# Kernel tuning notes

Hardware: AMD Instinct MI355X
Metric: run time of the kernel (lower is better)

## Reference

```python
import jax, jax.numpy as jnp
import numpy as np

TOP_K = 4  # num_experts_per_tok


def setup_inputs() -> dict:
    key = jax.random.key(0)
    ks = jax.random.split(key, 7)
    B, S, H, E, I = 1, 1024, 1024, 16, 2880
    scale_h = 1.0 / np.sqrt(H)
    scale_i = 1.0 / np.sqrt(I)
    return {
        "hidden_states": jax.random.normal(ks[0], (B, S, H), jnp.float32),
        "gate_w": jax.random.normal(ks[1], (E, H), jnp.float32) * scale_h,
        "gate_b": jax.random.normal(ks[2], (E,), jnp.float32) * 0.01,
        "gate_up_proj": jax.random.normal(ks[3], (E, H, 2 * I), jnp.float32) * scale_h,
        "gate_up_proj_bias": jax.random.normal(ks[4], (E, 2 * I), jnp.float32) * 0.01,
        "down_proj": jax.random.normal(ks[5], (E, I, H), jnp.float32) * scale_i,
        "down_proj_bias": jax.random.normal(ks[6], (E, H), jnp.float32) * 0.01,
    }


def reference(hidden_states, gate_w, gate_b, gate_up_proj, gate_up_proj_bias,
              down_proj, down_proj_bias):
    B, S, H = hidden_states.shape
    E = gate_w.shape[0]
    I = down_proj.shape[1]
    x = hidden_states.reshape(-1, H)  # [T, H]
    T = x.shape[0]

    # Router: top-k logits, softmax over selected logits only
    router_logits = x @ gate_w.T + gate_b          # [T, E]
    top_vals, top_idx = jax.lax.top_k(router_logits, TOP_K)
    routing_weights = jax.nn.softmax(top_vals, axis=-1)  # [T, K]

    # Combine matrix: C[t, e] = routing weight of expert e for token t (0 if unselected)
    C = jnp.zeros((T, E), x.dtype).at[jnp.arange(T)[:, None], top_idx].add(routing_weights)

    # Dense per-expert MLP (reference computes all experts, combine masks unselected)
    gu = jnp.einsum('th,ehf->tef', x, gate_up_proj) + gate_up_proj_bias[None]  # [T, E, 2I]
    gate, up = gu[..., :I], gu[..., I:]
    inter = jax.nn.silu(gate) * up                                            # [T, E, I]
    expert_out = jnp.einsum('tei,eih->teh', inter, down_proj) + down_proj_bias[None]  # [T, E, H]
    out = jnp.einsum('teh,te->th', expert_out, C)                             # [T, H]

    return out.reshape(B, S, H), router_logits
```

## Files before the change

### kernel.cpp

```cpp
#include <hip/hip_runtime.h>
#include <hip/hip_bf16.h>
#include <stdint.h>

#define T_TOK 1024
#define HDIM  1024
#define NEXP  16
#define IDIM  2880
#define GU_COLS (2*IDIM)
#define TOPK  4

using short4v  = __attribute__((ext_vector_type(4))) short;
using short8   = __attribute__((ext_vector_type(8))) short;
using ushort4v = __attribute__((ext_vector_type(4))) unsigned short;
using f32x4    = __attribute__((ext_vector_type(4))) float;

__device__ __forceinline__ unsigned short f2b(float f) {
    union { float f; unsigned u; } x; x.f = f;
    unsigned r = x.u + 0x7FFFu + ((x.u >> 16) & 1u);
    return (unsigned short)(r >> 16);
}

typedef const __attribute__((address_space(1))) unsigned int* gas1_t;
typedef __attribute__((address_space(3))) unsigned int* las3_t;
__device__ __forceinline__ void gload16(const void* g, void* l) {
    __builtin_amdgcn_global_load_lds((gas1_t)g, (las3_t)l, 16, 0, 0);
}

__global__ __launch_bounds__(256) void router_kernel(
    const float* __restrict__ x, const float* __restrict__ gw,
    const float* __restrict__ gb, float* __restrict__ logits_out,
    int* __restrict__ counts, int* __restrict__ lists, float* __restrict__ wts,
    unsigned short* __restrict__ xb, float* __restrict__ out)
{
    int t = blockIdx.x;
    int tid = threadIdx.x;
    const float* xr = x + (size_t)t * HDIM;
    {
        float4 v = *(const float4*)(xr + tid * 4);
        ushort4v b; b.x = f2b(v.x); b.y = f2b(v.y); b.z = f2b(v.z); b.w = f2b(v.w);
        *(ushort4v*)(xb + (size_t)t * HDIM + tid * 4) = b;
        float4 z = make_float4(0.f, 0.f, 0.f, 0.f);
        *(float4*)(out + (size_t)t * HDIM + tid * 4) = z;
    }
    int e = tid >> 4;
    int l16 = tid & 15;
    const float* wr = gw + (size_t)e * HDIM;
    float p = 0.f;
    for (int h = l16; h < HDIM; h += 16) p += xr[h] * wr[h];
    p += __shfl_xor(p, 8);
    p += __shfl_xor(p, 4);
    p += __shfl_xor(p, 2);
    p += __shfl_xor(p, 1);
    __shared__ float sl[NEXP];
    if (l16 == 0) {
        float v = p + gb[e];
        sl[e] = v;
        logits_out[t * NEXP + e] = v;
    }
    __syncthreads();
    if (tid == 0) {
        float v[NEXP];
#pragma unroll
        for (int i = 0; i < NEXP; ++i) v[i] = sl[i];
        int idx[TOPK]; float tv[TOPK];
        unsigned used = 0;
#pragma unroll
        for (int k = 0; k < TOPK; ++k) {
            float best = -__builtin_inff(); int bi = 0;
#pragma unroll
            for (int i = 0; i < NEXP; ++i)
                if (!((used >> i) & 1u) && v[i] > best) { best = v[i]; bi = i; }
            used |= 1u << bi; idx[k] = bi; tv[k] = best;
        }
        float m = tv[0];
        float ex[TOPK], s = 0.f;
#pragma unroll
        for (int k = 0; k < TOPK; ++k) { ex[k] = expf(tv[k] - m); s += ex[k]; }
#pragma unroll
        for (int k = 0; k < TOPK; ++k) {
            float w = ex[k] / s;
            int slot = atomicAdd(&counts[idx[k]], 1);
            lists[idx[k] * T_TOK + slot] = t;
            wts[idx[k] * T_TOK + slot] = w;
        }
    }
}

__global__ void offsets_kernel(const int* __restrict__ counts, int* __restrict__ offsets)
{
    if (threadIdx.x == 0) {
        int o = 0;
        for (int e = 0; e < NEXP; ++e) { offsets[e] = o; o += counts[e]; }
        offsets[NEXP] = o;
    }
}

__global__ __launch_bounds__(512) void gu_kernel(
    const unsigned short* __restrict__ xb, const float* __restrict__ gup,
    const float* __restrict__ gub, const int* __restrict__ counts,
    const int* __restrict__ offsets, const int* __restrict__ lists,
    unsigned short* __restrict__ inter)
{
    int bid = blockIdx.x;
    int nt = bid % 90;
    int t2 = bid / 90;
    int e  = t2 & 15;
    int mt = t2 >> 4;
    int ne = counts[e];
    if (mt * 256 >= ne) return;

    int tid = threadIdx.x;
    int wave = tid >> 6, lane = tid & 63;
    int l16 = lane & 15, lq = lane >> 4;

    __shared__ int tokid[256];
    __shared__ unsigned short As[256 * 64];
    __shared__ unsigned short Bs[64 * 64];

    if (tid < 256) {
        int slot = mt * 256 + tid;
        tokid[tid] = (slot < ne) ? lists[e * T_TOK + slot] : lists[e * T_TOK];
    }
    __syncthreads();

    const float* gup_e = gup + (size_t)e * HDIM * GU_COLS;

    int at = tid - 256;
    const unsigned short* asrc[8];
    if (tid >= 256) {
#pragma unroll
        for (int i = 0; i < 8; ++i) {
            int s = at + i * 256;
            int row = s >> 3, c = s & 7;
            asrc[i] = xb + (size_t)tokid[row] * HDIM + ((c ^ (row & 7)) * 8);
        }
    }
    int nb = tid & 15, kb = tid >> 4;
    const float* bsrc = nullptr;
    if (tid < 256) {
        int n0 = nb * 4;
        size_t col = (n0 < 32) ? (size_t)(nt * 32 + n0) : (size_t)(IDIM + nt * 32 + (n0 - 32));
        bsrc = gup_e + (size_t)(kb * 4) * GU_COLS + col;
    }

    f32x4 acc[2][4];
#pragma unroll
    for (int i = 0; i < 2; ++i)
#pragma unroll
        for (int f = 0; f < 4; ++f) acc[i][f] = (f32x4){0.f, 0.f, 0.f, 0.f};

    float4 br0, br1, br2, br3;
    if (tid < 256) {
        br0 = *(const float4*)(bsrc);
        br1 = *(const float4*)(bsrc + GU_COLS);
        br2 = *(const float4*)(bsrc + 2 * GU_COLS);
        br3 = *(const float4*)(bsrc + 3 * GU_COLS);
    }

    for (int kk = 0; kk < HDIM; kk += 64) {
        __syncthreads();
        if (tid >= 256) {
#pragma unroll
            for (int i = 0; i < 8; ++i)
                gload16(asrc[i] + kk, As + ((size_t)(at + i * 256)) * 8);
        } else {
#pragma unroll
            for (int j = 0; j < 4; ++j) {
                int n = nb * 4 + j;
                int slot = kb ^ (n & 15);
                ushort4v b;
                b.x = f2b((&br0.x)[j]); b.y = f2b((&br1.x)[j]);
                b.z = f2b((&br2.x)[j]); b.w = f2b((&br3.x)[j]);
                *(ushort4v*)&Bs[n * 64 + slot * 4] = b;
            }
        }
        __syncthreads();
        if (tid < 256 && kk + 64 < HDIM) {
            const float* sp = bsrc + (size_t)(kk + 64) * GU_COLS;
            br0 = *(const float4*)(sp);
            br1 = *(const float4*)(sp + GU_COLS);
            br2 = *(const float4*)(sp + 2 * GU_COLS);
            br3 = *(const float4*)(sp + 3 * GU_COLS);
        }
#pragma unroll
        for (int ks = 0; ks < 2; ++ks) {
            short8 a[2], b[4];
#pragma unroll
            for (int i = 0; i < 2; ++i) {
                int row = wave * 32 + i * 16 + l16;
                int q = ks * 4 + lq;
                a[i] = *(const short8*)&As[row * 64 + ((q ^ (row & 7)) * 8)];
            }
#pragma unroll
            for (int f = 0; f < 4; ++f) {
                int n = f * 16 + l16;
                int u0 = (ks * 8 + lq * 2) ^ (n & 15);
                int u1 = (ks * 8 + lq * 2 + 1) ^ (n & 15);
                short4v h0 = *(const short4v*)&Bs[n * 64 + u0 * 4];
                short4v h1 = *(const short4v*)&Bs[n * 64 + u1 * 4];
                b[f] = __builtin_shufflevector(h0, h1, 0, 1, 2, 3, 4, 5, 6, 7);
            }
#pragma unroll
            for (int i = 0; i < 2; ++i)
#pragma unroll
                for (int f = 0; f < 4; ++f)
                    acc[i][f] = __builtin_amdgcn_mfma_f32_16x16x32_bf16(a[i], b[f], acc[i][f], 0, 0, 0);
        }
    }

    int off = offsets[e];
    const float* gbe = gub + (size_t)e * GU_COLS;
#pragma unroll
    for (int j = 0; j < 2; ++j) {
        int col = j * 16 + l16;
        float bg = gbe[nt * 32 + col];
        float bu = gbe[IDIM + nt * 32 + col];
#pragma unroll
        for (int i = 0; i < 2; ++i)
#pragma unroll
            for (int r = 0; r < 4; ++r) {
                int row = wave * 32 + i * 16 + lq * 4 + r;
                int slot = mt * 256 + row;
                if (slot < ne) {
                    float g = acc[i][j][r] + bg;
                    float u = acc[i][j + 2][r] + bu;
                    float sg = g / (1.f + expf(-g));
                    inter[(size_t)(off + slot) * IDIM + nt * 32 + col] = f2b(sg * u);
                }
            }
    }
}

__global__ __launch_bounds__(512) void down_kernel(
    const unsigned short* __restrict__ inter, const float* __restrict__ dw,
    const float* __restrict__ db, const int* __restrict__ counts,
    const int* __restrict__ offsets, const int* __restrict__ lists,
    const float* __restrict__ wts, float* __restrict__ out)
{
    int bid = blockIdx.x;
    int ht = bid & 15;
    int t2 = bid >> 4;
    int e  = t2 & 15;
    int mt = t2 >> 4;
    int ne = counts[e];
    if (mt * 256 >= ne) return;

    int tid = threadIdx.x;
    int wave = tid >> 6, lane = tid & 63;
    int l16 = lane & 15, lq = lane >> 4;

    __shared__ int tokid[256];
    __shared__ float twt[256];
    __shared__ unsigned short As[256 * 64];
    __shared__ unsigned short Bs[64 * 64];

    int off = offsets[e];
    if (tid < 256) {
        int slot = mt * 256 + tid;
        tokid[tid] = (slot < ne) ? lists[e * T_TOK + slot] : -1;
        twt[tid]   = (slot < ne) ? wts[e * T_TOK + slot] : 0.f;
    }
    __syncthreads();

    const float* dw_e = dw + (size_t)e * IDIM * HDIM;

    int at = tid - 256;
    const unsigned short* asrc[8];
    if (tid >= 256) {
#pragma unroll
        for (int i = 0; i < 8; ++i) {
            int s = at + i * 256;
            int row = s >> 3, c = s & 7;
            int slotr = mt * 256 + row; if (slotr >= ne) slotr = ne - 1;
            asrc[i] = inter + (size_t)(off + slotr) * IDIM + ((c ^ (row & 7)) * 8);
        }
    }
    int nb = tid & 15, kb = tid >> 4;
    const float* bsrc = nullptr;
    if (tid < 256)
        bsrc = dw_e + (size_t)(kb * 4) * HDIM + ht * 64 + nb * 4;

    f32x4 acc[2][4];
#pragma unroll
    for (int i = 0; i < 2; ++i)
#pragma unroll
        for (int f = 0; f < 4; ++f) acc[i][f] = (f32x4){0.f, 0.f, 0.f, 0.f};

    float4 br0, br1, br2, br3;
    if (tid < 256) {
        br0 = *(const float4*)(bsrc);
        br1 = *(const float4*)(bsrc + HDIM);
        br2 = *(const float4*)(bsrc + 2 * HDIM);
        br3 = *(const float4*)(bsrc + 3 * HDIM);
    }

    for (int kk = 0; kk < IDIM; kk += 64) {
        __syncthreads();
        if (tid >= 256) {
#pragma unroll
            for (int i = 0; i < 8; ++i)
                gload16(asrc[i] + kk, As + ((size_t)(at + i * 256)) * 8);
        } else {
#pragma unroll
            for (int j = 0; j < 4; ++j) {
                int n = nb * 4 + j;
                int slot = kb ^ (n & 15);
                ushort4v b;
                b.x = f2b((&br0.x)[j]); b.y = f2b((&br1.x)[j]);
                b.z = f2b((&br2.x)[j]); b.w = f2b((&br3.x)[j]);
                *(ushort4v*)&Bs[n * 64 + slot * 4] = b;
            }
        }
        __syncthreads();
        if (tid < 256 && kk + 64 < IDIM) {
            const float* sp = bsrc + (size_t)(kk + 64) * HDIM;
            br0 = *(const float4*)(sp);
            br1 = *(const float4*)(sp + HDIM);
            br2 = *(const float4*)(sp + 2 * HDIM);
            br3 = *(const float4*)(sp + 3 * HDIM);
        }
#pragma unroll
        for (int ks = 0; ks < 2; ++ks) {
            short8 a[2], b[4];
#pragma unroll
            for (int i = 0; i < 2; ++i) {
                int row = wave * 32 + i * 16 + l16;
                int q = ks * 4 + lq;
                a[i] = *(const short8*)&As[row * 64 + ((q ^ (row & 7)) * 8)];
            }
#pragma unroll
            for (int f = 0; f < 4; ++f) {
                int n = f * 16 + l16;
                int u0 = (ks * 8 + lq * 2) ^ (n & 15);
                int u1 = (ks * 8 + lq * 2 + 1) ^ (n & 15);
                short4v h0 = *(const short4v*)&Bs[n * 64 + u0 * 4];
                short4v h1 = *(const short4v*)&Bs[n * 64 + u1 * 4];
                b[f] = __builtin_shufflevector(h0, h1, 0, 1, 2, 3, 4, 5, 6, 7);
            }
#pragma unroll
            for (int i = 0; i < 2; ++i)
#pragma unroll
                for (int f = 0; f < 4; ++f)
                    acc[i][f] = __builtin_amdgcn_mfma_f32_16x16x32_bf16(a[i], b[f], acc[i][f], 0, 0, 0);
        }
    }

    const float* db_e = db + (size_t)e * HDIM;
#pragma unroll
    for (int f = 0; f < 4; ++f) {
        int h = ht * 64 + f * 16 + l16;
        float bias = db_e[h];
#pragma unroll
        for (int i = 0; i < 2; ++i)
#pragma unroll
            for (int r = 0; r < 4; ++r) {
                int row = wave * 32 + i * 16 + lq * 4 + r;
                int tk = tokid[row];
                if (tk >= 0)
                    atomicAdd(out + (size_t)tk * HDIM + h, twt[row] * (acc[i][f][r] + bias));
            }
    }
}

extern "C" void kernel_launch(void* const* d_in, const int* in_sizes, int n_in,
                              void* d_out, int out_size, void* d_ws, size_t ws_size,
                              hipStream_t stream)
{
    const float* x   = (const float*)d_in[0];
    const float* gw  = (const float*)d_in[1];
    const float* gb  = (const float*)d_in[2];
    const float* gup = (const float*)d_in[3];
    const float* gub = (const float*)d_in[4];
    const float* dw  = (const float*)d_in[5];
    const float* db  = (const float*)d_in[6];

    float* out        = (float*)d_out;
    float* logits_out = out + (size_t)T_TOK * HDIM;

    char* ws = (char*)d_ws;
    int*   counts  = (int*)(ws + 0);
    int*   offsets = (int*)(ws + 256);
    int*   lists   = (int*)(ws + 512);
    float* wts     = (float*)(ws + 512 + 65536);
    unsigned short* xb    = (unsigned short*)(ws + 131584);
    unsigned short* inter = (unsigned short*)(ws + 2228736);

    hipMemsetAsync(counts, 0, 64, stream);

    router_kernel<<<T_TOK, 256, 0, stream>>>(x, gw, gb, logits_out, counts, lists, wts, xb, out);
    offsets_kernel<<<1, 64, 0, stream>>>(counts, offsets);
    gu_kernel<<<4 * NEXP * 90, 512, 0, stream>>>(xb, gup, gub, counts, offsets, lists, inter);
    down_kernel<<<4 * NEXP * 16, 512, 0, stream>>>(inter, dw, db, counts, offsets, lists, wts, out);
}
```

Before: 307.5 us.

## Double N-tile width in MoE GEMMs to 128 with 4x2 wave layout

Widens the per-block N tile from 64 to 128 columns in both the gate/up and down expert GEMMs. Waves are rearranged into a 4x2 grid so each computes a 64x64 sub-tile, which halves the grid size and the number of times the gathered activation tile is reloaded. Raises MFMA priority around the compute loop with s_setprio. In exchange it uses more accumulator registers and LDS per block and launches fewer blocks, which can lower occupancy and leave some CUs idle.

```diff
diff --git a/kernel.cpp b/kernel.cpp
--- a/kernel.cpp
+++ b/kernel.cpp
@@ -102,8 +102,8 @@
     unsigned short* __restrict__ inter)
 {
     int bid = blockIdx.x;
-    int nt = bid % 90;
-    int t2 = bid / 90;
+    int nt = bid % 45;
+    int t2 = bid / 45;
     int e  = t2 & 15;
     int mt = t2 >> 4;
     int ne = counts[e];
@@ -112,10 +112,11 @@
     int tid = threadIdx.x;
     int wave = tid >> 6, lane = tid & 63;
     int l16 = lane & 15, lq = lane >> 4;
+    int wm = wave >> 1, wn = wave & 1;
 
     __shared__ int tokid[256];
     __shared__ unsigned short As[256 * 64];
-    __shared__ unsigned short Bs[64 * 64];
+    __shared__ unsigned short Bs[128 * 64];
 
     if (tid < 256) {
         int slot = mt * 256 + tid;
@@ -136,25 +137,31 @@
         }
     }
     int nb = tid & 15, kb = tid >> 4;
-    const float* bsrc = nullptr;
-    if (tid < 256) {
-        int n0 = nb * 4;
-        size_t col = (n0 < 32) ? (size_t)(nt * 32 + n0) : (size_t)(IDIM + nt * 32 + (n0 - 32));
-        bsrc = gup_e + (size_t)(kb * 4) * GU_COLS + col;
-    }
-
-    f32x4 acc[2][4];
-#pragma unroll
-    for (int i = 0; i < 2; ++i)
+    const float* bsrcg[2];
+    if (tid < 256) {
+#pragma unroll
+        for (int t = 0; t < 2; ++t) {
+            int n0 = (nb + t * 16) * 4;
+            int is_up = (n0 >> 5) & 1;
+            int cw = (n0 & 31) + ((n0 >> 6) << 5);
+            size_t gcol = (is_up ? (size_t)IDIM : 0) + (size_t)nt * 64 + cw;
+            bsrcg[t] = gup_e + (size_t)(kb * 4) * GU_COLS + gcol;
+        }
+    }
+
+    f32x4 acc[4][4];
+#pragma unroll
+    for (int i = 0; i < 4; ++i)
 #pragma unroll
         for (int f = 0; f < 4; ++f) acc[i][f] = (f32x4){0.f, 0.f, 0.f, 0.f};
 
-    float4 br0, br1, br2, br3;
-    if (tid < 256) {
-        br0 = *(const float4*)(bsrc);
-        br1 = *(const float4*)(bsrc + GU_COLS);
-        br2 = *(const float4*)(bsrc + 2 * GU_COLS);
-        br3 = *(const float4*)(bsrc + 3 * GU_COLS);
+    float4 br[2][4];
+    if (tid < 256) {
+#pragma unroll
+        for (int t = 0; t < 2; ++t)
+#pragma unroll
+            for (int k = 0; k < 4; ++k)
+                br[t][k] = *(const float4*)(bsrcg[t] + (size_t)k * GU_COLS);
     }
 
     for (int kk = 0; kk < HDIM; kk += 64) {
@@ -165,67 +172,71 @@
                 gload16(asrc[i] + kk, As + ((size_t)(at + i * 256)) * 8);
         } else {
 #pragma unroll
-            for (int j = 0; j < 4; ++j) {
-                int n = nb * 4 + j;
-                int slot = kb ^ (n & 15);
-                ushort4v b;
-                b.x = f2b((&br0.x)[j]); b.y = f2b((&br1.x)[j]);
-                b.z = f2b((&br2.x)[j]); b.w = f2b((&br3.x)[j]);
-                *(ushort4v*)&Bs[n * 64 + slot * 4] = b;
-            }
+            for (int t = 0; t < 2; ++t)
+#pragma unroll
+                for (int j = 0; j < 4; ++j) {
+                    int n = (nb + t * 16) * 4 + j;
+                    int slot = kb ^ (n & 15);
+                    ushort4v b;
+                    b.x = f2b((&br[t][0].x)[j]); b.y = f2b((&br[t][1].x)[j]);
+                    b.z = f2b((&br[t][2].x)[j]); b.w = f2b((&br[t][3].x)[j]);
+                    *(ushort4v*)&Bs[n * 64 + slot * 4] = b;
+                }
         }
         __syncthreads();
         if (tid < 256 && kk + 64 < HDIM) {
-            const float* sp = bsrc + (size_t)(kk + 64) * GU_COLS;
-            br0 = *(const float4*)(sp);
-            br1 = *(const float4*)(sp + GU_COLS);
-            br2 = *(const float4*)(sp + 2 * GU_COLS);
-            br3 = *(const float4*)(sp + 3 * GU_COLS);
-        }
+#pragma unroll
+            for (int t = 0; t < 2; ++t)
+#pragma unroll
+                for (int k = 0; k < 4; ++k)
+                    br[t][k] = *(const float4*)(bsrcg[t] + (size_t)(kk + 64 + k) * GU_COLS);
+        }
+        __builtin_amdgcn_s_setprio(1);
 #pragma unroll
         for (int ks = 0; ks < 2; ++ks) {
-            short8 a[2], b[4];
-#pragma unroll
-            for (int i = 0; i < 2; ++i) {
-                int row = wave * 32 + i * 16 + l16;
+            short8 a[4], b[4];
+#pragma unroll
+            for (int i = 0; i < 4; ++i) {
+                int row = wm * 64 + i * 16 + l16;
                 int q = ks * 4 + lq;
                 a[i] = *(const short8*)&As[row * 64 + ((q ^ (row & 7)) * 8)];
             }
 #pragma unroll
             for (int f = 0; f < 4; ++f) {
-                int n = f * 16 + l16;
-                int u0 = (ks * 8 + lq * 2) ^ (n & 15);
-                int u1 = (ks * 8 + lq * 2 + 1) ^ (n & 15);
+                int n = wn * 64 + f * 16 + l16;
+                int u0 = (ks * 8 + lq * 2) ^ l16;
+                int u1 = (ks * 8 + lq * 2 + 1) ^ l16;
                 short4v h0 = *(const short4v*)&Bs[n * 64 + u0 * 4];
                 short4v h1 = *(const short4v*)&Bs[n * 64 + u1 * 4];
                 b[f] = __builtin_shufflevector(h0, h1, 0, 1, 2, 3, 4, 5, 6, 7);
             }
 #pragma unroll
-            for (int i = 0; i < 2; ++i)
+            for (int i = 0; i < 4; ++i)
 #pragma unroll
                 for (int f = 0; f < 4; ++f)
                     acc[i][f] = __builtin_amdgcn_mfma_f32_16x16x32_bf16(a[i], b[f], acc[i][f], 0, 0, 0);
         }
+        __builtin_amdgcn_s_setprio(0);
     }
 
     int off = offsets[e];
     const float* gbe = gub + (size_t)e * GU_COLS;
 #pragma unroll
     for (int j = 0; j < 2; ++j) {
-        int col = j * 16 + l16;
-        float bg = gbe[nt * 32 + col];
-        float bu = gbe[IDIM + nt * 32 + col];
-#pragma unroll
-        for (int i = 0; i < 2; ++i)
+        int cw = wn * 32 + j * 16 + l16;
+        float bg = gbe[nt * 64 + cw];
+        float bu = gbe[IDIM + nt * 64 + cw];
+#pragma unroll
+        for (int i = 0; i < 4; ++i)
 #pragma unroll
             for (int r = 0; r < 4; ++r) {
-                int row = wave * 32 + i * 16 + lq * 4 + r;
+                int row = wm * 64 + i * 16 + lq * 4 + r;
                 int slot = mt * 256 + row;
                 if (slot < ne) {
                     float g = acc[i][j][r] + bg;
                     float u = acc[i][j + 2][r] + bu;
                     float sg = g / (1.f + expf(-g));
-                    inter[(size_t)(off + slot) * IDIM + nt * 32 + col] = f2b(sg * u);
+                    inter[(size_t)(off + slot) * IDIM + nt * 64 + cw] = f2b(sg * u);
                 }
             }
     }
@@ -238,8 +249,8 @@
     const float* __restrict__ wts, float* __restrict__ out)
 {
     int bid = blockIdx.x;
-    int ht = bid & 15;
-    int t2 = bid >> 4;
+    int ht = bid & 7;
+    int t2 = bid >> 3;
     int e  = t2 & 15;
     int mt = t2 >> 4;
     int ne = counts[e];
@@ -248,11 +259,12 @@
     int tid = threadIdx.x;
     int wave = tid >> 6, lane = tid & 63;
     int l16 = lane & 15, lq = lane >> 4;
+    int wm = wave >> 1, wn = wave & 1;
 
     __shared__ int tokid[256];
     __shared__ float twt[256];
     __shared__ unsigned short As[256 * 64];
-    __shared__ unsigned short Bs[64 * 64];
+    __shared__ unsigned short Bs[128 * 64];
 
     int off = offsets[e];
     if (tid < 256) {
@@ -276,22 +288,26 @@
         }
     }
     int nb = tid & 15, kb = tid >> 4;
-    const float* bsrc = nullptr;
-    if (tid < 256)
-        bsrc = dw_e + (size_t)(kb * 4) * HDIM + ht * 64 + nb * 4;
-
-    f32x4 acc[2][4];
-#pragma unroll
-    for (int i = 0; i < 2; ++i)
+    const float* bsrcg[2];
+    if (tid < 256) {
+#pragma unroll
+        for (int t = 0; t < 2; ++t)
+            bsrcg[t] = dw_e + (size_t)(kb * 4) * HDIM + ht * 128 + (nb + t * 16) * 4;
+    }
+
+    f32x4 acc[4][4];
+#pragma unroll
+    for (int i = 0; i < 4; ++i)
 #pragma unroll
         for (int f = 0; f < 4; ++f) acc[i][f] = (f32x4){0.f, 0.f, 0.f, 0.f};
 
-    float4 br0, br1, br2, br3;
-    if (tid < 256) {
-        br0 = *(const float4*)(bsrc);
-        br1 = *(const float4*)(bsrc + HDIM);
-        br2 = *(const float4*)(bsrc + 2 * HDIM);
-        br3 = *(const float4*)(bsrc + 3 * HDIM);
+    float4 br[2][4];
+    if (tid < 256) {
+#pragma unroll
+        for (int t = 0; t < 2; ++t)
+#pragma unroll
+            for (int k = 0; k < 4; ++k)
+                br[t][k] = *(const float4*)(bsrcg[t] + (size_t)k * HDIM);
     }
 
     for (int kk = 0; kk < IDIM; kk += 64) {
@@ -302,59 +318,63 @@
                 gload16(asrc[i] + kk, As + ((size_t)(at + i * 256)) * 8);
         } else {
 #pragma unroll
-            for (int j = 0; j < 4; ++j) {
-                int n = nb * 4 + j;
-                int slot = kb ^ (n & 15);
-                ushort4v b;
-                b.x = f2b((&br0.x)[j]); b.y = f2b((&br1.x)[j]);
-                b.z = f2b((&br2.x)[j]); b.w = f2b((&br3.x)[j]);
-                *(ushort4v*)&Bs[n * 64 + slot * 4] = b;
-            }
+            for (int t = 0; t < 2; ++t)
+#pragma unroll
+                for (int j = 0; j < 4; ++j) {
+                    int n = (nb + t * 16) * 4 + j;
+                    int slot = kb ^ (n & 15);
+                    ushort4v b;
+                    b.x = f2b((&br[t][0].x)[j]); b.y = f2b((&br[t][1].x)[j]);
+                    b.z = f2b((&br[t][2].x)[j]); b.w = f2b((&br[t][3].x)[j]);
+                    *(ushort4v*)&Bs[n * 64 + slot * 4] = b;
+                }
         }
         __syncthreads();
         if (tid < 256 && kk + 64 < IDIM) {
-            const float* sp = bsrc + (size_t)(kk + 64) * HDIM;
-            br0 = *(const float4*)(sp);
-            br1 = *(const float4*)(sp + HDIM);
-            br2 = *(const float4*)(sp + 2 * HDIM);
-            br3 = *(const float4*)(sp + 3 * HDIM);
-        }
+#pragma unroll
+            for (int t = 0; t < 2; ++t)
+#pragma unroll
+                for (int k = 0; k < 4; ++k)
+                    br[t][k] = *(const float4*)(bsrcg[t] + (size_t)(kk + 64 + k) * HDIM);
+        }
+        __builtin_amdgcn_s_setprio(1);
 #pragma unroll
         for (int ks = 0; ks < 2; ++ks) {
-            short8 a[2], b[4];
-#pragma unroll
-            for (int i = 0; i < 2; ++i) {
-                int row = wave * 32 + i * 16 + l16;
+            short8 a[4], b[4];
+#pragma unroll
+            for (int i = 0; i < 4; ++i) {
+                int row = wm * 64 + i * 16 + l16;
                 int q = ks * 4 + lq;
                 a[i] = *(const short8*)&As[row * 64 + ((q ^ (row & 7)) * 8)];
             }
 #pragma unroll
             for (int f = 0; f < 4; ++f) {
-                int n = f * 16 + l16;
-                int u0 = (ks * 8 + lq * 2) ^ (n & 15);
-                int u1 = (ks * 8 + lq * 2 + 1) ^ (n & 15);
+                int n = wn * 64 + f * 16 + l16;
+                int u0 = (ks * 8 + lq * 2) ^ l16;
+                int u1 = (ks * 8 + lq * 2 + 1) ^ l16;
                 short4v h0 = *(const short4v*)&Bs[n * 64 + u0 * 4];
                 short4v h1 = *(const short4v*)&Bs[n * 64 + u1 * 4];
                 b[f] = __builtin_shufflevector(h0, h1, 0, 1, 2, 3, 4, 5, 6, 7);
             }
 #pragma unroll
-            for (int i = 0; i < 2; ++i)
+            for (int i = 0; i < 4; ++i)
 #pragma unroll
                 for (int f = 0; f < 4; ++f)
                     acc[i][f] = __builtin_amdgcn_mfma_f32_16x16x32_bf16(a[i], b[f], acc[i][f], 0, 0, 0);
         }
+        __builtin_amdgcn_s_setprio(0);
     }
 
     const float* db_e = db + (size_t)e * HDIM;
 #pragma unroll
     for (int f = 0; f < 4; ++f) {
-        int h = ht * 64 + f * 16 + l16;
+        int h = ht * 128 + wn * 64 + f * 16 + l16;
         float bias = db_e[h];
 #pragma unroll
-        for (int i = 0; i < 2; ++i)
+        for (int i = 0; i < 4; ++i)
 #pragma unroll
             for (int r = 0; r < 4; ++r) {
-                int row = wave * 32 + i * 16 + lq * 4 + r;
+                int row = wm * 64 + i * 16 + lq * 4 + r;
                 int tk = tokid[row];
                 if (tk >= 0)
                     atomicAdd(out + (size_t)tk * HDIM + h, twt[row] * (acc[i][f][r] + bias));
@@ -389,6 +409,6 @@
 
     router_kernel<<<T_TOK, 256, 0, stream>>>(x, gw, gb, logits_out, counts, lists, wts, xb, out);
     offsets_kernel<<<1, 64, 0, stream>>>(counts, offsets);
-    gu_kernel<<<4 * NEXP * 90, 512, 0, stream>>>(xb, gup, gub, counts, offsets, lists, inter);
-    down_kernel<<<4 * NEXP * 16, 512, 0, stream>>>(inter, dw, db, counts, offsets, lists, wts, out);
-}
+    gu_kernel<<<4 * NEXP * 45, 512, 0, stream>>>(xb, gup, gub, counts, offsets, lists, inter);
+    down_kernel<<<4 * NEXP * 8, 512, 0, stream>>>(inter, dw, db, counts, offsets, lists, wts, out);
+}
```

New measurement: 346.9 us. 12.8% more time.

## Split down-proj K dimension across two blocks, widen LDS B reads, raise MFMA priority

Applied to the files above, without the earlier changes.

The down-projection kernel now splits the 2880-long reduction into two halves handled by separate blocks, doubling the grid. Both halves accumulate into the output with atomics, and only the first half adds the bias. The aim is more parallelism for the down GEMM, at the cost of twice as many output atomics and duplicate A-tile loads per block. The B-tile swizzle is changed to XOR with (n&14) so each lane can fetch its B fragment with one 16-byte LDS read instead of two 8-byte reads. s_setprio is raised around the MFMA section in both GEMM kernels.

```diff
diff --git a/kernel.cpp b/kernel.cpp
--- a/kernel.cpp
+++ b/kernel.cpp
@@ -9,7 +9,6 @@
 #define GU_COLS (2*IDIM)
 #define TOPK  4
 
-using short4v  = __attribute__((ext_vector_type(4))) short;
 using short8   = __attribute__((ext_vector_type(8))) short;
 using ushort4v = __attribute__((ext_vector_type(4))) unsigned short;
 using f32x4    = __attribute__((ext_vector_type(4))) float;
@@ -167,7 +166,7 @@
 #pragma unroll
             for (int j = 0; j < 4; ++j) {
                 int n = nb * 4 + j;
-                int slot = kb ^ (n & 15);
+                int slot = kb ^ (n & 14);
                 ushort4v b;
                 b.x = f2b((&br0.x)[j]); b.y = f2b((&br1.x)[j]);
                 b.z = f2b((&br2.x)[j]); b.w = f2b((&br3.x)[j]);
@@ -182,6 +181,7 @@
             br2 = *(const float4*)(sp + 2 * GU_COLS);
             br3 = *(const float4*)(sp + 3 * GU_COLS);
         }
+        __builtin_amdgcn_s_setprio(1);
 #pragma unroll
         for (int ks = 0; ks < 2; ++ks) {
             short8 a[2], b[4];
@@ -194,11 +194,8 @@
 #pragma unroll
             for (int f = 0; f < 4; ++f) {
                 int n = f * 16 + l16;
-                int u0 = (ks * 8 + lq * 2) ^ (n & 15);
-                int u1 = (ks * 8 + lq * 2 + 1) ^ (n & 15);
-                short4v h0 = *(const short4v*)&Bs[n * 64 + u0 * 4];
-                short4v h1 = *(const short4v*)&Bs[n * 64 + u1 * 4];
-                b[f] = __builtin_shufflevector(h0, h1, 0, 1, 2, 3, 4, 5, 6, 7);
+                int u = (ks * 8 + lq * 2) ^ (n & 14);
+                b[f] = *(const short8*)&Bs[n * 64 + u * 4];
             }
 #pragma unroll
             for (int i = 0; i < 2; ++i)
@@ -206,6 +203,7 @@
                 for (int f = 0; f < 4; ++f)
                     acc[i][f] = __builtin_amdgcn_mfma_f32_16x16x32_bf16(a[i], b[f], acc[i][f], 0, 0, 0);
         }
+        __builtin_amdgcn_s_setprio(0);
     }
 
     int off = offsets[e];
@@ -238,12 +236,15 @@
     const float* __restrict__ wts, float* __restrict__ out)
 {
     int bid = blockIdx.x;
-    int ht = bid & 15;
-    int t2 = bid >> 4;
-    int e  = t2 & 15;
-    int mt = t2 >> 4;
+    int ht  = bid & 15;
+    int e   = (bid >> 4) & 15;
+    int ksp = (bid >> 8) & 1;
+    int mt  = bid >> 9;
     int ne = counts[e];
     if (mt * 256 >= ne) return;
+
+    int k0   = ksp * 1472;
+    int kend = ksp ? IDIM : 1472;
 
     int tid = threadIdx.x;
     int wave = tid >> 6, lane = tid & 63;
@@ -288,13 +289,14 @@
 
     float4 br0, br1, br2, br3;
     if (tid < 256) {
-        br0 = *(const float4*)(bsrc);
-        br1 = *(const float4*)(bsrc + HDIM);
-        br2 = *(const float4*)(bsrc + 2 * HDIM);
-        br3 = *(const float4*)(bsrc + 3 * HDIM);
-    }
-
-    for (int kk = 0; kk < IDIM; kk += 64) {
+        const float* sp = bsrc + (size_t)k0 * HDIM;
+        br0 = *(const float4*)(sp);
+        br1 = *(const float4*)(sp + HDIM);
+        br2 = *(const float4*)(sp + 2 * HDIM);
+        br3 = *(const float4*)(sp + 3 * HDIM);
+    }
+
+    for (int kk = k0; kk < kend; kk += 64) {
         __syncthreads();
         if (tid >= 256) {
 #pragma unroll
@@ -304,7 +306,7 @@
 #pragma unroll
             for (int j = 0; j < 4; ++j) {
                 int n = nb * 4 + j;
-                int slot = kb ^ (n & 15);
+                int slot = kb ^ (n & 14);
                 ushort4v b;
                 b.x = f2b((&br0.x)[j]); b.y = f2b((&br1.x)[j]);
                 b.z = f2b((&br2.x)[j]); b.w = f2b((&br3.x)[j]);
@@ -312,13 +314,14 @@
             }
         }
         __syncthreads();
-        if (tid < 256 && kk + 64 < IDIM) {
+        if (tid < 256 && kk + 64 < kend) {
             const float* sp = bsrc + (size_t)(kk + 64) * HDIM;
             br0 = *(const float4*)(sp);
             br1 = *(const float4*)(sp + HDIM);
             br2 = *(const float4*)(sp + 2 * HDIM);
             br3 = *(const float4*)(sp + 3 * HDIM);
         }
+        __builtin_amdgcn_s_setprio(1);
 #pragma unroll
         for (int ks = 0; ks < 2; ++ks) {
             short8 a[2], b[4];
@@ -331,11 +334,8 @@
 #pragma unroll
             for (int f = 0; f < 4; ++f) {
                 int n = f * 16 + l16;
-                int u0 = (ks * 8 + lq * 2) ^ (n & 15);
-                int u1 = (ks * 8 + lq * 2 + 1) ^ (n & 15);
-                short4v h0 = *(const short4v*)&Bs[n * 64 + u0 * 4];
-                short4v h1 = *(const short4v*)&Bs[n * 64 + u1 * 4];
-                b[f] = __builtin_shufflevector(h0, h1, 0, 1, 2, 3, 4, 5, 6, 7);
+                int u = (ks * 8 + lq * 2) ^ (n & 14);
+                b[f] = *(const short8*)&Bs[n * 64 + u * 4];
             }
 #pragma unroll
             for (int i = 0; i < 2; ++i)
@@ -343,13 +343,14 @@
                 for (int f = 0; f < 4; ++f)
                     acc[i][f] = __builtin_amdgcn_mfma_f32_16x16x32_bf16(a[i], b[f], acc[i][f], 0, 0, 0);
         }
+        __builtin_amdgcn_s_setprio(0);
     }
 
     const float* db_e = db + (size_t)e * HDIM;
 #pragma unroll
     for (int f = 0; f < 4; ++f) {
         int h = ht * 64 + f * 16 + l16;
-        float bias = db_e[h];
+        float bias = (ksp == 0) ? db_e[h] : 0.f;
 #pragma unroll
         for (int i = 0; i < 2; ++i)
 #pragma unroll
@@ -390,5 +391,5 @@
     router_kernel<<<T_TOK, 256, 0, stream>>>(x, gw, gb, logits_out, counts, lists, wts, xb, out);
     offsets_kernel<<<1, 64, 0, stream>>>(counts, offsets);
     gu_kernel<<<4 * NEXP * 90, 512, 0, stream>>>(xb, gup, gub, counts, offsets, lists, inter);
-    down_kernel<<<4 * NEXP * 16, 512, 0, stream>>>(inter, dw, db, counts, offsets, lists, wts, out);
-}
+    down_kernel<<<4 * 2 * NEXP * 16, 512, 0, stream>>>(inter, dw, db, counts, offsets, lists, wts, out);
+}
```

Measured after the change: 334.4 us. +8.8%, slower.

## Replace atomic scatter in down projection with per-slot stores and gather kernel

Applied to the files above, without the earlier changes.

The down kernel now writes each expert's un-weighted output rows into a contiguous fp32 buffer instead of atomically adding weighted results into the output. A new gather kernel reads each token's four expert rows via recorded (expert, slot) pairs and forms the weighted sum. This removes the output zeroing and the float atomics, at the cost of an extra ~16MB write plus read and one more launch. It also raises wave priority around the MFMA loops in both GEMM kernels.

```diff
diff --git a/kernel.cpp b/kernel.cpp
--- a/kernel.cpp
+++ b/kernel.cpp
@@ -30,7 +30,8 @@
     const float* __restrict__ x, const float* __restrict__ gw,
     const float* __restrict__ gb, float* __restrict__ logits_out,
     int* __restrict__ counts, int* __restrict__ lists, float* __restrict__ wts,
-    unsigned short* __restrict__ xb, float* __restrict__ out)
+    int* __restrict__ tokslot4, float* __restrict__ wts4,
+    unsigned short* __restrict__ xb)
 {
     int t = blockIdx.x;
     int tid = threadIdx.x;
@@ -39,8 +40,6 @@
         float4 v = *(const float4*)(xr + tid * 4);
         ushort4v b; b.x = f2b(v.x); b.y = f2b(v.y); b.z = f2b(v.z); b.w = f2b(v.w);
         *(ushort4v*)(xb + (size_t)t * HDIM + tid * 4) = b;
-        float4 z = make_float4(0.f, 0.f, 0.f, 0.f);
-        *(float4*)(out + (size_t)t * HDIM + tid * 4) = z;
     }
     int e = tid >> 4;
     int l16 = tid & 15;
@@ -82,6 +81,8 @@
             int slot = atomicAdd(&counts[idx[k]], 1);
             lists[idx[k] * T_TOK + slot] = t;
             wts[idx[k] * T_TOK + slot] = w;
+            tokslot4[t * TOPK + k] = (idx[k] << 16) | slot;
+            wts4[t * TOPK + k] = w;
         }
     }
 }
@@ -182,6 +183,7 @@
             br2 = *(const float4*)(sp + 2 * GU_COLS);
             br3 = *(const float4*)(sp + 3 * GU_COLS);
         }
+        __builtin_amdgcn_s_setprio(1);
 #pragma unroll
         for (int ks = 0; ks < 2; ++ks) {
             short8 a[2], b[4];
@@ -206,6 +208,7 @@
                 for (int f = 0; f < 4; ++f)
                     acc[i][f] = __builtin_amdgcn_mfma_f32_16x16x32_bf16(a[i], b[f], acc[i][f], 0, 0, 0);
         }
+        __builtin_amdgcn_s_setprio(0);
     }
 
     int off = offsets[e];
@@ -234,14 +237,12 @@
 __global__ __launch_bounds__(512) void down_kernel(
     const unsigned short* __restrict__ inter, const float* __restrict__ dw,
     const float* __restrict__ db, const int* __restrict__ counts,
-    const int* __restrict__ offsets, const int* __restrict__ lists,
-    const float* __restrict__ wts, float* __restrict__ out)
+    const int* __restrict__ offsets, float* __restrict__ eo)
 {
     int bid = blockIdx.x;
-    int ht = bid & 15;
-    int t2 = bid >> 4;
-    int e  = t2 & 15;
-    int mt = t2 >> 4;
+    int ht  = bid & 15;
+    int e   = (bid >> 4) & 15;
+    int mt  = bid >> 8;
     int ne = counts[e];
     if (mt * 256 >= ne) return;
 
@@ -249,18 +250,10 @@
     int wave = tid >> 6, lane = tid & 63;
     int l16 = lane & 15, lq = lane >> 4;
 
-    __shared__ int tokid[256];
-    __shared__ float twt[256];
     __shared__ unsigned short As[256 * 64];
     __shared__ unsigned short Bs[64 * 64];
 
     int off = offsets[e];
-    if (tid < 256) {
-        int slot = mt * 256 + tid;
-        tokid[tid] = (slot < ne) ? lists[e * T_TOK + slot] : -1;
-        twt[tid]   = (slot < ne) ? wts[e * T_TOK + slot] : 0.f;
-    }
-    __syncthreads();
 
     const float* dw_e = dw + (size_t)e * IDIM * HDIM;
 
@@ -319,6 +312,7 @@
             br2 = *(const float4*)(sp + 2 * HDIM);
             br3 = *(const float4*)(sp + 3 * HDIM);
         }
+        __builtin_amdgcn_s_setprio(1);
 #pragma unroll
         for (int ks = 0; ks < 2; ++ks) {
             short8 a[2], b[4];
@@ -343,6 +337,7 @@
                 for (int f = 0; f < 4; ++f)
                     acc[i][f] = __builtin_amdgcn_mfma_f32_16x16x32_bf16(a[i], b[f], acc[i][f], 0, 0, 0);
         }
+        __builtin_amdgcn_s_setprio(0);
     }
 
     const float* db_e = db + (size_t)e * HDIM;
@@ -355,11 +350,37 @@
 #pragma unroll
             for (int r = 0; r < 4; ++r) {
                 int row = wave * 32 + i * 16 + lq * 4 + r;
-                int tk = tokid[row];
-                if (tk >= 0)
-                    atomicAdd(out + (size_t)tk * HDIM + h, twt[row] * (acc[i][f][r] + bias));
-            }
-    }
+                int slot = mt * 256 + row;
+                if (slot < ne)
+                    eo[(size_t)(off + slot) * HDIM + h] = acc[i][f][r] + bias;
+            }
+    }
+}
+
+__global__ __launch_bounds__(256) void gather_kernel(
+    const float* __restrict__ eo, const int* __restrict__ tokslot4,
+    const float* __restrict__ wts4, const int* __restrict__ offsets,
+    float* __restrict__ out)
+{
+    int t = blockIdx.x;
+    int tid = threadIdx.x;
+    int rows[TOPK]; float w[TOPK];
+#pragma unroll
+    for (int k = 0; k < TOPK; ++k) {
+        int ts = tokslot4[t * TOPK + k];
+        int e = ts >> 16, slot = ts & 0xFFFF;
+        rows[k] = offsets[e] + slot;
+        w[k] = wts4[t * TOPK + k];
+    }
+    int h0 = tid * 4;
+    float4 s = make_float4(0.f, 0.f, 0.f, 0.f);
+#pragma unroll
+    for (int k = 0; k < TOPK; ++k) {
+        float4 v = *(const float4*)(eo + (size_t)rows[k] * HDIM + h0);
+        s.x += w[k] * v.x; s.y += w[k] * v.y;
+        s.z += w[k] * v.z; s.w += w[k] * v.w;
+    }
+    *(float4*)(out + (size_t)t * HDIM + h0) = s;
 }
 
 extern "C" void kernel_launch(void* const* d_in, const int* in_sizes, int n_in,
@@ -378,17 +399,21 @@
     float* logits_out = out + (size_t)T_TOK * HDIM;
 
     char* ws = (char*)d_ws;
-    int*   counts  = (int*)(ws + 0);
-    int*   offsets = (int*)(ws + 256);
-    int*   lists   = (int*)(ws + 512);
-    float* wts     = (float*)(ws + 512 + 65536);
-    unsigned short* xb    = (unsigned short*)(ws + 131584);
-    unsigned short* inter = (unsigned short*)(ws + 2228736);
+    int*   counts   = (int*)(ws + 0);
+    int*   offsets  = (int*)(ws + 256);
+    int*   lists    = (int*)(ws + 512);
+    float* wts      = (float*)(ws + 512 + 65536);
+    int*   tokslot4 = (int*)(ws + 512 + 131072);
+    float* wts4     = (float*)(ws + 512 + 131072 + 16384);
+    unsigned short* xb    = (unsigned short*)(ws + 164352);
+    unsigned short* inter = (unsigned short*)(ws + 2261504);
+    float*          eo    = (float*)(ws + 25854464);
 
     hipMemsetAsync(counts, 0, 64, stream);
 
-    router_kernel<<<T_TOK, 256, 0, stream>>>(x, gw, gb, logits_out, counts, lists, wts, xb, out);
+    router_kernel<<<T_TOK, 256, 0, stream>>>(x, gw, gb, logits_out, counts, lists, wts, tokslot4, wts4, xb);
     offsets_kernel<<<1, 64, 0, stream>>>(counts, offsets);
     gu_kernel<<<4 * NEXP * 90, 512, 0, stream>>>(xb, gup, gub, counts, offsets, lists, inter);
-    down_kernel<<<4 * NEXP * 16, 512, 0, stream>>>(inter, dw, db, counts, offsets, lists, wts, out);
-}
+    down_kernel<<<4 * NEXP * 16, 512, 0, stream>>>(inter, dw, db, counts, offsets, eo);
+    gather_kernel<<<T_TOK, 256, 0, stream>>>(eo, tokslot4, wts4, offsets, out);
+}
```

Result: no change. 306.4 us (-0.4%).
